# Optimization experiments

Measured on AMD Instinct MI355X. Metric: run time of the kernel, lower is better.

Reference implementation:

```python
import jax, jax.numpy as jnp
import numpy as np

B, S, E = 4, 2048, 512
H = 8          # 'layers' = number of heads
DK, DV = 64, 64
DK_H, DV_H = DK // H, DV // H  # = 8 each


def setup_inputs() -> dict:
    key = jax.random.key(0)
    ks = jax.random.split(key, 8)
    scale = 1.0 / np.sqrt(E)
    return {
        "query": jax.random.normal(ks[0], (B, S, E), jnp.float32),
        "key": jax.random.normal(ks[1], (B, S, E), jnp.float32),
        "value": jax.random.normal(ks[2], (B, S, E), jnp.float32),
        "padding_mask": jnp.ones((B, S, S), dtype=bool),
        "decoder_mask": 1,
        # stacked per-head projection weights (nn.Linear, bias=False)
        "Wq": jax.random.normal(ks[3], (H, E, DK_H), jnp.float32) * scale,
        "Wk": jax.random.normal(ks[4], (H, E, DK_H), jnp.float32) * scale,
        "Wv": jax.random.normal(ks[5], (H, E, DV_H), jnp.float32) * scale,
        # output projection: Linear(dV -> embed_size) with bias
        "Wo": jax.random.normal(ks[6], (DV, E), jnp.float32) * (1.0 / np.sqrt(DV)),
        "bo": jax.random.normal(ks[7], (E,), jnp.float32) * 0.01,
    }


def reference(query, key, value, padding_mask, decoder_mask, Wq, Wk, Wv, Wo, bo):
    # Batched over all heads at once (same math as the per-head Python loop).
    Q = jnp.einsum("bse,hed->bhsd", query, Wq)   # [B,H,S,dk_h]
    K = jnp.einsum("bse,hed->bhsd", key, Wk)
    V = jnp.einsum("bse,hed->bhsd", value, Wv)
    s = jnp.einsum("bhsd,bhtd->bhst", Q, K)      # [B,H,S,S] raw scores
    if decoder_mask:
        # faithful to: where(tril(scores)==0.0, -inf, scores)
        s = jnp.where(jnp.tril(s) == 0.0, -jnp.inf, s)
    # masked_fill(~padding_mask, -inf), broadcast over heads
    s = jnp.where(padding_mask[:, None, :, :], s, -jnp.inf)
    # note: scaling happens AFTER masking in the original (-inf stays -inf)
    s = s / jnp.sqrt(jnp.float32(DK_H))
    a = jax.nn.softmax(s, axis=-1)
    # dropout in eval mode -> identity
    o = jnp.einsum("bhst,bhtd->bhsd", a, V)      # [B,H,S,dv_h]
    o = o.transpose(0, 2, 1, 3).reshape(o.shape[0], o.shape[2], H * DV_H)  # concat heads
    return o @ Wo + bo                            # output projection (dropout = identity)
```

## Files before the change

kernel.cpp:

```cpp
#include <hip/hip_runtime.h>

#define BB 4
#define SS 2048
#define EE 512
#define HH 8
#define DHH 8
#define DVV 64

#define NEG (-1e30f)

__global__ __launch_bounds__(256)
void proj_kernel(const float* __restrict__ q, const float* __restrict__ k,
                 const float* __restrict__ v,
                 const float* __restrict__ Wq, const float* __restrict__ Wk,
                 const float* __restrict__ Wv,
                 float* __restrict__ Qp, float* __restrict__ Kp,
                 float* __restrict__ Vp)
{
  const float* x; const float* W; float* outp;
  if (blockIdx.y == 0)      { x = q; W = Wq; outp = Qp; }
  else if (blockIdx.y == 1) { x = k; W = Wk; outp = Kp; }
  else                      { x = v; W = Wv; outp = Vp; }

  __shared__ float Xs[64][68];
  __shared__ float Ws[64][68];

  int t = threadIdx.x;
  int row0 = blockIdx.x * 64;
  int tr = t >> 4;
  int tc = t & 15;

  float acc[4][4];
  #pragma unroll
  for (int i = 0; i < 4; i++)
    #pragma unroll
    for (int j = 0; j < 4; j++) acc[i][j] = 0.f;

  for (int kt = 0; kt < EE/64; kt++) {
    __syncthreads();
    {
      int row = t >> 2;
      #pragma unroll
      for (int it = 0; it < 4; it++) {
        int kq = 4*it + (t & 3);
        float4 vv = *(const float4*)(x + (size_t)(row0+row)*EE + kt*64 + 4*kq);
        Xs[4*kq+0][row] = vv.x;
        Xs[4*kq+1][row] = vv.y;
        Xs[4*kq+2][row] = vv.z;
        Xs[4*kq+3][row] = vv.w;
      }
    }
    #pragma unroll
    for (int it = 0; it < 4; it++) {
      int lin = t + 256*it;
      int kk  = lin >> 4;
      int rem = lin & 15;
      int h   = rem >> 1;
      int dq  = rem & 1;
      float4 vv = *(const float4*)(W + (size_t)h*EE*DHH + (size_t)(kt*64+kk)*DHH + dq*4);
      *(float4*)&Ws[kk][h*8 + dq*4] = vv;
    }
    __syncthreads();

    #pragma unroll 8
    for (int kk = 0; kk < 64; kk++) {
      float4 a = *(const float4*)&Xs[kk][4*tr];
      float4 bq = *(const float4*)&Ws[kk][4*tc];
      float av[4] = {a.x, a.y, a.z, a.w};
      float bv[4] = {bq.x, bq.y, bq.z, bq.w};
      #pragma unroll
      for (int i = 0; i < 4; i++)
        #pragma unroll
        for (int j = 0; j < 4; j++) acc[i][j] += av[i] * bv[j];
    }
  }

  int h = tc >> 1, dbase = (tc & 1) * 4;
  #pragma unroll
  for (int i = 0; i < 4; i++) {
    int row = row0 + 4*tr + i;
    int b = row >> 11, s = row & (SS - 1);
    float4 vv; vv.x = acc[i][0]; vv.y = acc[i][1]; vv.z = acc[i][2]; vv.w = acc[i][3];
    *(float4*)(outp + (((size_t)b*HH + h)*SS + s)*DHH + dbase) = vv;
  }
}

__global__ __launch_bounds__(256, 2)
void attn_kernel(const float* __restrict__ Qp, const float* __restrict__ Kp,
                 const float* __restrict__ Vp, float* __restrict__ O)
{
  int bx = blockIdx.x, h = blockIdx.y, b = blockIdx.z;
  const float* Qh = Qp + (((size_t)b*HH + h)*SS)*DHH;
  const float* Kh = Kp + (((size_t)b*HH + h)*SS)*DHH;
  const float* Vh = Vp + (((size_t)b*HH + h)*SS)*DHH;

  __shared__ float Ks[2][128*DHH];
  __shared__ float Vs[2][128*DHH];
  __shared__ float Ps[4*64*10];

  const int t  = threadIdx.x;
  const int rg = t & 15;
  const int cs = t >> 4;
  const float SCL = 0.35355339059327373f * 1.4426950408889634f;

  int cur = 0;

  for (int pass = 0; pass < 2; pass++) {
    const int qb = (pass == 0) ? bx : (31 - bx);
    const int row0t = qb*64 + 4*rg;

    float qreg[4][8];
    #pragma unroll
    for (int i = 0; i < 4; i++) {
      const float* qp = Qh + (size_t)(row0t + i) * DHH;
      float4 a = *(const float4*)qp;
      float4 c = *(const float4*)(qp + 4);
      qreg[i][0] = a.x*SCL; qreg[i][1] = a.y*SCL;
      qreg[i][2] = a.z*SCL; qreg[i][3] = a.w*SCL;
      qreg[i][4] = c.x*SCL; qreg[i][5] = c.y*SCL;
      qreg[i][6] = c.z*SCL; qreg[i][7] = c.w*SCL;
    }

    float M = 0.f, negM = 0.f;
    float l[4];
    float o[4][8];
    #pragma unroll
    for (int i = 0; i < 4; i++) {
      l[i] = 0.f;
      #pragma unroll
      for (int d = 0; d < 8; d++) o[i][d] = 0.f;
    }

    ((float4*)Ks[cur])[t] = ((const float4*)Kh)[t];
    ((float4*)Vs[cur])[t] = ((const float4*)Vh)[t];

    const int ktd = qb >> 1;
    for (int kt = 0; kt <= ktd; kt++) {
      __syncthreads();
      float4 kstg, vstg;
      const bool pre = (kt < ktd);
      if (pre) {
        kstg = ((const float4*)(Kh + (size_t)(kt+1)*128*DHH))[t];
        vstg = ((const float4*)(Vh + (size_t)(kt+1)*128*DHH))[t];
      }
      const float* KsC = Ks[cur];
      const float* VsC = Vs[cur];

      if (kt < ktd) {
        #pragma unroll
        for (int j = 0; j < 8; j++) {
          const int c8 = (cs + 16*j) * DHH;
          float4 k0 = *(const float4*)&KsC[c8];
          float4 k1 = *(const float4*)&KsC[c8 + 4];
          float4 v0 = *(const float4*)&VsC[c8];
          float4 v1 = *(const float4*)&VsC[c8 + 4];
          #pragma unroll
          for (int i = 0; i < 4; i++) {
            float s = fmaf(qreg[i][0], k0.x, negM);
            s = fmaf(qreg[i][1], k0.y, s);
            s = fmaf(qreg[i][2], k0.z, s);
            s = fmaf(qreg[i][3], k0.w, s);
            s = fmaf(qreg[i][4], k1.x, s);
            s = fmaf(qreg[i][5], k1.y, s);
            s = fmaf(qreg[i][6], k1.z, s);
            s = fmaf(qreg[i][7], k1.w, s);
            const float p = __builtin_amdgcn_exp2f(s);
            l[i] += p;
            o[i][0] = fmaf(p, v0.x, o[i][0]);
            o[i][1] = fmaf(p, v0.y, o[i][1]);
            o[i][2] = fmaf(p, v0.z, o[i][2]);
            o[i][3] = fmaf(p, v0.w, o[i][3]);
            o[i][4] = fmaf(p, v1.x, o[i][4]);
            o[i][5] = fmaf(p, v1.y, o[i][5]);
            o[i][6] = fmaf(p, v1.z, o[i][6]);
            o[i][7] = fmaf(p, v1.w, o[i][7]);
          }
        }
      } else {
        #pragma unroll
        for (int j = 0; j < 8; j++) {
          const int c  = cs + 16*j;
          const int cg = kt*128 + c;
          if (cg > row0t + 3) break;
          const int c8 = c * DHH;
          float4 k0 = *(const float4*)&KsC[c8];
          float4 k1 = *(const float4*)&KsC[c8 + 4];
          float4 v0 = *(const float4*)&VsC[c8];
          float4 v1 = *(const float4*)&VsC[c8 + 4];
          #pragma unroll
          for (int i = 0; i < 4; i++) {
            float s = fmaf(qreg[i][0], k0.x, negM);
            s = fmaf(qreg[i][1], k0.y, s);
            s = fmaf(qreg[i][2], k0.z, s);
            s = fmaf(qreg[i][3], k0.w, s);
            s = fmaf(qreg[i][4], k1.x, s);
            s = fmaf(qreg[i][5], k1.y, s);
            s = fmaf(qreg[i][6], k1.z, s);
            s = fmaf(qreg[i][7], k1.w, s);
            s = (cg > row0t + i) ? NEG : s;
            const float p = __builtin_amdgcn_exp2f(s);
            l[i] += p;
            o[i][0] = fmaf(p, v0.x, o[i][0]);
            o[i][1] = fmaf(p, v0.y, o[i][1]);
            o[i][2] = fmaf(p, v0.z, o[i][2]);
            o[i][3] = fmaf(p, v0.w, o[i][3]);
            o[i][4] = fmaf(p, v1.x, o[i][4]);
            o[i][5] = fmaf(p, v1.y, o[i][5]);
            o[i][6] = fmaf(p, v1.z, o[i][6]);
            o[i][7] = fmaf(p, v1.w, o[i][7]);
          }
        }
      }

      float lm = fmaxf(fmaxf(l[0], l[1]), fmaxf(l[2], l[3]));
      if (__any(lm > 1e18f)) {
        const float dsc = 5.421010862427522e-20f;
        #pragma unroll
        for (int i = 0; i < 4; i++) {
          l[i] *= dsc;
          #pragma unroll
          for (int d = 0; d < 8; d++) o[i][d] *= dsc;
        }
        M += 64.f; negM = -M;
      }

      if (pre) {
        ((float4*)Ks[cur ^ 1])[t] = kstg;
        ((float4*)Vs[cur ^ 1])[t] = vstg;
        cur ^= 1;
      }
    }

    #pragma unroll
    for (int i = 0; i < 4; i++) {
      l[i] += __shfl_xor(l[i], 16);
      #pragma unroll
      for (int d = 0; d < 8; d++) o[i][d] += __shfl_xor(o[i][d], 16);
      l[i] += __shfl_xor(l[i], 32);
      #pragma unroll
      for (int d = 0; d < 8; d++) o[i][d] += __shfl_xor(o[i][d], 32);
    }

    if ((t & 48) == 0) {
      const int w = t >> 6;
      #pragma unroll
      for (int i = 0; i < 4; i++) {
        float* ps = &Ps[(size_t)(w*64 + 4*rg + i) * 10];
        ps[0] = M; ps[1] = l[i];
        #pragma unroll
        for (int d = 0; d < 8; d++) ps[2 + d] = o[i][d];
      }
    }
    __syncthreads();

    if (t < 64) {
      float Mx = NEG, L = 0.f;
      float O8[8] = {0,0,0,0,0,0,0,0};
      #pragma unroll
      for (int ww = 0; ww < 4; ww++) {
        const float* ps = &Ps[(size_t)(ww*64 + t) * 10];
        const float mo = ps[0], lo = ps[1];
        const float mm = fmaxf(Mx, mo);
        const float a1 = __builtin_amdgcn_exp2f(Mx - mm);
        const float a2 = __builtin_amdgcn_exp2f(mo - mm);
        L = L*a1 + lo*a2;
        #pragma unroll
        for (int d = 0; d < 8; d++) O8[d] = O8[d]*a1 + ps[2 + d]*a2;
        Mx = mm;
      }
      const float inv = 1.0f / L;
      const int qrow = qb*64 + t;
      float* dst = O + ((size_t)b*SS + qrow)*DVV + h*DHH;
      float4 w0, w1;
      w0.x = O8[0]*inv; w0.y = O8[1]*inv; w0.z = O8[2]*inv; w0.w = O8[3]*inv;
      w1.x = O8[4]*inv; w1.y = O8[5]*inv; w1.z = O8[6]*inv; w1.w = O8[7]*inv;
      *(float4*)dst = w0;
      *(float4*)(dst + 4) = w1;
    }
  }
}

__global__ __launch_bounds__(256)
void outproj_kernel(const float* __restrict__ Oin, const float* __restrict__ Wo,
                    const float* __restrict__ bo, float* __restrict__ out)
{
  __shared__ float Os[64][68];
  int t = threadIdx.x;
  int row0 = blockIdx.x * 64;
  int col0 = blockIdx.y * 128;

  {
    int row = t >> 2;
    #pragma unroll
    for (int it = 0; it < 4; it++) {
      int kq = 4*it + (t & 3);
      float4 vv = *(const float4*)(Oin + (size_t)(row0+row)*DVV + 4*kq);
      Os[4*kq+0][row] = vv.x;
      Os[4*kq+1][row] = vv.y;
      Os[4*kq+2][row] = vv.z;
      Os[4*kq+3][row] = vv.w;
    }
  }
  __syncthreads();

  int rg = t >> 5;
  int tc = t & 31;
  const float* wp = Wo + col0 + 4*tc;
  float4 b4 = *(const float4*)(bo + col0 + 4*tc);

  float acc[8][4];
  #pragma unroll
  for (int r = 0; r < 8; r++) {
    acc[r][0] = b4.x; acc[r][1] = b4.y; acc[r][2] = b4.z; acc[r][3] = b4.w;
  }

  #pragma unroll 8
  for (int k = 0; k < DVV; k++) {
    float4 w = *(const float4*)(wp + (size_t)k*EE);
    float xr[8];
    *(float4*)&xr[0] = *(const float4*)&Os[k][8*rg];
    *(float4*)&xr[4] = *(const float4*)&Os[k][8*rg + 4];
    #pragma unroll
    for (int r = 0; r < 8; r++) {
      acc[r][0] += xr[r]*w.x;
      acc[r][1] += xr[r]*w.y;
      acc[r][2] += xr[r]*w.z;
      acc[r][3] += xr[r]*w.w;
    }
  }

  #pragma unroll
  for (int r = 0; r < 8; r++) {
    int row = row0 + 8*rg + r;
    float4 vv; vv.x = acc[r][0]; vv.y = acc[r][1]; vv.z = acc[r][2]; vv.w = acc[r][3];
    *(float4*)(out + (size_t)row*EE + col0 + 4*tc) = vv;
  }
}

extern "C" void kernel_launch(void* const* d_in, const int* in_sizes, int n_in,
                              void* d_out, int out_size, void* d_ws, size_t ws_size,
                              hipStream_t stream) {
  const void* qkv[3] = {nullptr, nullptr, nullptr};
  const void* Wlist[4] = {nullptr, nullptr, nullptr, nullptr};
  const void* bo = nullptr;
  int nqkv = 0, nw = 0;
  for (int i = 0; i < n_in; i++) {
    int sz = in_sizes[i];
    if (sz == BB*SS*EE)            { if (nqkv < 3) qkv[nqkv] = d_in[i]; nqkv++; }
    else if (sz == HH*EE*DHH)      { if (nw < 4) Wlist[nw] = d_in[i]; nw++; }
    else if (sz == EE)             { bo = d_in[i]; }
  }
  float* out = (float*)d_out;

  float* Qp = (float*)d_ws;
  float* Kp = Qp + (size_t)BB*HH*SS*DHH;
  float* Vp = Kp + (size_t)BB*HH*SS*DHH;
  float* O  = Vp + (size_t)BB*HH*SS*DHH;

  dim3 gA(BB*SS/64, 3, 1);
  proj_kernel<<<gA, 256, 0, stream>>>((const float*)qkv[0], (const float*)qkv[1],
                                      (const float*)qkv[2],
                                      (const float*)Wlist[0], (const float*)Wlist[1],
                                      (const float*)Wlist[2], Qp, Kp, Vp);

  dim3 gB(16, HH, BB);
  attn_kernel<<<gB, 256, 0, stream>>>(Qp, Kp, Vp, O);

  dim3 gC(BB*SS/64, EE/128, 1);
  outproj_kernel<<<gC, 256, 0, stream>>>(O, (const float*)Wlist[3],
                                         (const float*)bo, out);
}
```

Baseline: 220.7 us.

## Double-buffer projection GEMM tiles and remap threads to row-per-lane layout

The projection kernel now double-buffers its X and W shared-memory tiles, prefetching the next k-tile into registers while computing on the current one. The per-thread mapping also changes: each lane owns one row and each wave computes 16 output columns. The wave reads W as a broadcast and writes two full 8-float head outputs per thread. This hides global-load latency and drops one barrier per iteration, at the cost of doubled LDS use and more registers.

```diff
diff --git a/kernel.cpp b/kernel.cpp
--- a/kernel.cpp
+++ b/kernel.cpp
@@ -22,67 +22,122 @@
   else if (blockIdx.y == 1) { x = k; W = Wk; outp = Kp; }
   else                      { x = v; W = Wv; outp = Vp; }
 
-  __shared__ float Xs[64][68];
-  __shared__ float Ws[64][68];
-
-  int t = threadIdx.x;
-  int row0 = blockIdx.x * 64;
-  int tr = t >> 4;
-  int tc = t & 15;
-
-  float acc[4][4];
+  __shared__ float Xs[2][64][68];
+  __shared__ float Ws[2][64][68];
+
+  const int t    = threadIdx.x;
+  const int lane = t & 63;
+  const int wv   = t >> 6;
+  const int row0 = blockIdx.x * 64;
+
+  const int srow = t >> 2;
+
+  float acc[16];
   #pragma unroll
-  for (int i = 0; i < 4; i++)
-    #pragma unroll
-    for (int j = 0; j < 4; j++) acc[i][j] = 0.f;
-
+  for (int i = 0; i < 16; i++) acc[i] = 0.f;
+
+  float4 xv[4], wvv[4];
+
+  #pragma unroll
+  for (int it = 0; it < 4; it++) {
+    int kq = 4*it + (t & 3);
+    xv[it] = *(const float4*)(x + (size_t)(row0 + srow)*EE + 4*kq);
+    int lin = t + 256*it;
+    int kk  = lin >> 4;
+    int rem = lin & 15;
+    int h   = rem >> 1;
+    int dq  = rem & 1;
+    wvv[it] = *(const float4*)(W + (size_t)h*EE*DHH + (size_t)kk*DHH + dq*4);
+  }
+  #pragma unroll
+  for (int it = 0; it < 4; it++) {
+    int kq = 4*it + (t & 3);
+    Xs[0][4*kq+0][srow] = xv[it].x;
+    Xs[0][4*kq+1][srow] = xv[it].y;
+    Xs[0][4*kq+2][srow] = xv[it].z;
+    Xs[0][4*kq+3][srow] = xv[it].w;
+    int lin = t + 256*it;
+    int kk  = lin >> 4;
+    int rem = lin & 15;
+    int h   = rem >> 1;
+    int dq  = rem & 1;
+    *(float4*)&Ws[0][kk][h*8 + dq*4] = wvv[it];
+  }
+
+  int cur = 0;
   for (int kt = 0; kt < EE/64; kt++) {
     __syncthreads();
-    {
-      int row = t >> 2;
+    const bool pre = (kt < EE/64 - 1);
+    if (pre) {
       #pragma unroll
       for (int it = 0; it < 4; it++) {
         int kq = 4*it + (t & 3);
-        float4 vv = *(const float4*)(x + (size_t)(row0+row)*EE + kt*64 + 4*kq);
-        Xs[4*kq+0][row] = vv.x;
-        Xs[4*kq+1][row] = vv.y;
-        Xs[4*kq+2][row] = vv.z;
-        Xs[4*kq+3][row] = vv.w;
-      }
-    }
-    #pragma unroll
-    for (int it = 0; it < 4; it++) {
-      int lin = t + 256*it;
-      int kk  = lin >> 4;
-      int rem = lin & 15;
-      int h   = rem >> 1;
-      int dq  = rem & 1;
-      float4 vv = *(const float4*)(W + (size_t)h*EE*DHH + (size_t)(kt*64+kk)*DHH + dq*4);
-      *(float4*)&Ws[kk][h*8 + dq*4] = vv;
-    }
-    __syncthreads();
+        xv[it] = *(const float4*)(x + (size_t)(row0 + srow)*EE + (kt+1)*64 + 4*kq);
+        int lin = t + 256*it;
+        int kk  = lin >> 4;
+        int rem = lin & 15;
+        int h   = rem >> 1;
+        int dq  = rem & 1;
+        wvv[it] = *(const float4*)(W + (size_t)h*EE*DHH + (size_t)((kt+1)*64 + kk)*DHH + dq*4);
+      }
+    }
 
     #pragma unroll 8
     for (int kk = 0; kk < 64; kk++) {
-      float4 a = *(const float4*)&Xs[kk][4*tr];
-      float4 bq = *(const float4*)&Ws[kk][4*tc];
-      float av[4] = {a.x, a.y, a.z, a.w};
-      float bv[4] = {bq.x, bq.y, bq.z, bq.w};
-      #pragma unroll
-      for (int i = 0; i < 4; i++)
-        #pragma unroll
-        for (int j = 0; j < 4; j++) acc[i][j] += av[i] * bv[j];
-    }
-  }
-
-  int h = tc >> 1, dbase = (tc & 1) * 4;
-  #pragma unroll
-  for (int i = 0; i < 4; i++) {
-    int row = row0 + 4*tr + i;
-    int b = row >> 11, s = row & (SS - 1);
-    float4 vv; vv.x = acc[i][0]; vv.y = acc[i][1]; vv.z = acc[i][2]; vv.w = acc[i][3];
-    *(float4*)(outp + (((size_t)b*HH + h)*SS + s)*DHH + dbase) = vv;
-  }
+      float a = Xs[cur][kk][lane];
+      float4 w0 = *(const float4*)&Ws[cur][kk][16*wv + 0];
+      float4 w1 = *(const float4*)&Ws[cur][kk][16*wv + 4];
+      float4 w2 = *(const float4*)&Ws[cur][kk][16*wv + 8];
+      float4 w3 = *(const float4*)&Ws[cur][kk][16*wv + 12];
+      acc[0]  = fmaf(a, w0.x, acc[0]);
+      acc[1]  = fmaf(a, w0.y, acc[1]);
+      acc[2]  = fmaf(a, w0.z, acc[2]);
+      acc[3]  = fmaf(a, w0.w, acc[3]);
+      acc[4]  = fmaf(a, w1.x, acc[4]);
+      acc[5]  = fmaf(a, w1.y, acc[5]);
+      acc[6]  = fmaf(a, w1.z, acc[6]);
+      acc[7]  = fmaf(a, w1.w, acc[7]);
+      acc[8]  = fmaf(a, w2.x, acc[8]);
+      acc[9]  = fmaf(a, w2.y, acc[9]);
+      acc[10] = fmaf(a, w2.z, acc[10]);
+      acc[11] = fmaf(a, w2.w, acc[11]);
+      acc[12] = fmaf(a, w3.x, acc[12]);
+      acc[13] = fmaf(a, w3.y, acc[13]);
+      acc[14] = fmaf(a, w3.z, acc[14]);
+      acc[15] = fmaf(a, w3.w, acc[15]);
+    }
+
+    if (pre) {
+      #pragma unroll
+      for (int it = 0; it < 4; it++) {
+        int kq = 4*it + (t & 3);
+        Xs[cur^1][4*kq+0][srow] = xv[it].x;
+        Xs[cur^1][4*kq+1][srow] = xv[it].y;
+        Xs[cur^1][4*kq+2][srow] = xv[it].z;
+        Xs[cur^1][4*kq+3][srow] = xv[it].w;
+        int lin = t + 256*it;
+        int kk  = lin >> 4;
+        int rem = lin & 15;
+        int h   = rem >> 1;
+        int dq  = rem & 1;
+        *(float4*)&Ws[cur^1][kk][h*8 + dq*4] = wvv[it];
+      }
+      cur ^= 1;
+    }
+  }
+
+  const int grow = row0 + lane;
+  const int b = grow >> 11, s = grow & (SS - 1);
+  const int h0 = 2*wv, h1 = 2*wv + 1;
+  float* p0 = outp + (((size_t)b*HH + h0)*SS + s)*DHH;
+  float* p1 = outp + (((size_t)b*HH + h1)*SS + s)*DHH;
+  float4 o0, o1, o2, o3;
+  o0.x = acc[0];  o0.y = acc[1];  o0.z = acc[2];  o0.w = acc[3];
+  o1.x = acc[4];  o1.y = acc[5];  o1.z = acc[6];  o1.w = acc[7];
+  o2.x = acc[8];  o2.y = acc[9];  o2.z = acc[10]; o2.w = acc[11];
+  o3.x = acc[12]; o3.y = acc[13]; o3.z = acc[14]; o3.w = acc[15];
+  *(float4*)p0 = o0; *(float4*)(p0 + 4) = o1;
+  *(float4*)p1 = o2; *(float4*)(p1 + 4) = o3;
 }
 
 __global__ __launch_bounds__(256, 2)
```

Measured after the change: 229.3 us. 3.9% more time.

## Double-buffer X tile in projection kernel and read weights directly from global

Applied to the files above, without the earlier changes.

In the QKV projection kernel, the X tile is now double-buffered in shared memory with register prefetch of the next K-slice, so global loads overlap with compute and one barrier per iteration is removed. The weight tile is no longer staged in shared memory; each thread reads its float4 of weights straight from global (L1/L2 cached) inside the inner loop. This trades shared-memory traffic and a barrier for more global/cache load instructions in the hot loop. The projection is a small share of the total time next to attention, so the overall effect is likely limited.

```diff
diff --git a/kernel.cpp b/kernel.cpp
--- a/kernel.cpp
+++ b/kernel.cpp
@@ -22,13 +22,15 @@
   else if (blockIdx.y == 1) { x = k; W = Wk; outp = Kp; }
   else                      { x = v; W = Wv; outp = Vp; }
 
-  __shared__ float Xs[64][68];
-  __shared__ float Ws[64][68];
-
-  int t = threadIdx.x;
-  int row0 = blockIdx.x * 64;
-  int tr = t >> 4;
-  int tc = t & 15;
+  __shared__ float Xs[2][64][68];
+
+  const int t    = threadIdx.x;
+  const int row0 = blockIdx.x * 64;
+  const int tr = t >> 4;
+  const int tc = t & 15;
+  const int srow = t >> 2;
+
+  const float* wp = W + (size_t)(tc >> 1)*EE*DHH + (size_t)(tc & 1)*4;
 
   float acc[4][4];
   #pragma unroll
@@ -36,46 +38,72 @@
     #pragma unroll
     for (int j = 0; j < 4; j++) acc[i][j] = 0.f;
 
+  float4 xv[4];
+
+  #pragma unroll
+  for (int it = 0; it < 4; it++) {
+    int kq = 4*it + (t & 3);
+    xv[it] = *(const float4*)(x + (size_t)(row0 + srow)*EE + 4*kq);
+  }
+  #pragma unroll
+  for (int it = 0; it < 4; it++) {
+    int kq = 4*it + (t & 3);
+    Xs[0][4*kq+0][srow] = xv[it].x;
+    Xs[0][4*kq+1][srow] = xv[it].y;
+    Xs[0][4*kq+2][srow] = xv[it].z;
+    Xs[0][4*kq+3][srow] = xv[it].w;
+  }
+
+  int cur = 0;
   for (int kt = 0; kt < EE/64; kt++) {
     __syncthreads();
-    {
-      int row = t >> 2;
+    const bool pre = (kt < EE/64 - 1);
+    if (pre) {
       #pragma unroll
       for (int it = 0; it < 4; it++) {
         int kq = 4*it + (t & 3);
-        float4 vv = *(const float4*)(x + (size_t)(row0+row)*EE + kt*64 + 4*kq);
-        Xs[4*kq+0][row] = vv.x;
-        Xs[4*kq+1][row] = vv.y;
-        Xs[4*kq+2][row] = vv.z;
-        Xs[4*kq+3][row] = vv.w;
-      }
-    }
-    #pragma unroll
-    for (int it = 0; it < 4; it++) {
-      int lin = t + 256*it;
-      int kk  = lin >> 4;
-      int rem = lin & 15;
-      int h   = rem >> 1;
-      int dq  = rem & 1;
-      float4 vv = *(const float4*)(W + (size_t)h*EE*DHH + (size_t)(kt*64+kk)*DHH + dq*4);
-      *(float4*)&Ws[kk][h*8 + dq*4] = vv;
-    }
-    __syncthreads();
-
+        xv[it] = *(const float4*)(x + (size_t)(row0 + srow)*EE + (kt+1)*64 + 4*kq);
+      }
+    }
+
+    const float* wk = wp + (size_t)(kt*64)*DHH;
     #pragma unroll 8
     for (int kk = 0; kk < 64; kk++) {
-      float4 a = *(const float4*)&Xs[kk][4*tr];
-      float4 bq = *(const float4*)&Ws[kk][4*tc];
+      float4 a = *(const float4*)&Xs[cur][kk][4*tr];
+      float4 w = *(const float4*)(wk + (size_t)kk*DHH);
       float av[4] = {a.x, a.y, a.z, a.w};
-      float bv[4] = {bq.x, bq.y, bq.z, bq.w};
-      #pragma unroll
-      for (int i = 0; i < 4; i++)
-        #pragma unroll
-        for (int j = 0; j < 4; j++) acc[i][j] += av[i] * bv[j];
-    }
-  }
-
-  int h = tc >> 1, dbase = (tc & 1) * 4;
+      acc[0][0] = fmaf(av[0], w.x, acc[0][0]);
+      acc[0][1] = fmaf(av[0], w.y, acc[0][1]);
+      acc[0][2] = fmaf(av[0], w.z, acc[0][2]);
+      acc[0][3] = fmaf(av[0], w.w, acc[0][3]);
+      acc[1][0] = fmaf(av[1], w.x, acc[1][0]);
+      acc[1][1] = fmaf(av[1], w.y, acc[1][1]);
+      acc[1][2] = fmaf(av[1], w.z, acc[1][2]);
+      acc[1][3] = fmaf(av[1], w.w, acc[1][3]);
+      acc[2][0] = fmaf(av[2], w.x, acc[2][0]);
+      acc[2][1] = fmaf(av[2], w.y, acc[2][1]);
+      acc[2][2] = fmaf(av[2], w.z, acc[2][2]);
+      acc[2][3] = fmaf(av[2], w.w, acc[2][3]);
+      acc[3][0] = fmaf(av[3], w.x, acc[3][0]);
+      acc[3][1] = fmaf(av[3], w.y, acc[3][1]);
+      acc[3][2] = fmaf(av[3], w.z, acc[3][2]);
+      acc[3][3] = fmaf(av[3], w.w, acc[3][3]);
+    }
+
+    if (pre) {
+      #pragma unroll
+      for (int it = 0; it < 4; it++) {
+        int kq = 4*it + (t & 3);
+        Xs[cur^1][4*kq+0][srow] = xv[it].x;
+        Xs[cur^1][4*kq+1][srow] = xv[it].y;
+        Xs[cur^1][4*kq+2][srow] = xv[it].z;
+        Xs[cur^1][4*kq+3][srow] = xv[it].w;
+      }
+      cur ^= 1;
+    }
+  }
+
+  const int h = tc >> 1, dbase = (tc & 1) * 4;
   #pragma unroll
   for (int i = 0; i < 4; i++) {
     int row = row0 + 4*tr + i;
```

Result: slower. 251.4 us (+13.9%).

## Fuse projection, attention and output projection into one persistent kernel with grid barriers

Applied to the files above, without the earlier changes.

Merges the three kernel launches into a single 512-block kernel that runs the QKV projection, causal attention and output projection in turn, separated by atomic-counter grid barriers. Shared memory is overlaid through a union, and a memset clears the counter before each launch. The aim is to remove the launch gaps and tail effects between stages. In exchange it adds global barrier spin cost, relies on all 512 blocks being co-resident (2 per CU on 256 CUs) or it can deadlock, and adds a memset call.

```diff
diff --git a/kernel.cpp b/kernel.cpp
--- a/kernel.cpp
+++ b/kernel.cpp
@@ -9,331 +9,349 @@
 
 #define NEG (-1e30f)
 
-__global__ __launch_bounds__(256)
-void proj_kernel(const float* __restrict__ q, const float* __restrict__ k,
-                 const float* __restrict__ v,
-                 const float* __restrict__ Wq, const float* __restrict__ Wk,
-                 const float* __restrict__ Wv,
-                 float* __restrict__ Qp, float* __restrict__ Kp,
-                 float* __restrict__ Vp)
+
+union SharedU {
+  struct { float Xs[64][68]; float Ws[64][68]; } pj;
+  struct { float Ks[2][128*DHH]; float Vs[2][128*DHH]; float Ps[4*64*10]; } at;
+  struct { float Os[64][68]; } op;
+};
+
+__device__ __forceinline__ void grid_barrier(unsigned* cnt, unsigned target) {
+  __syncthreads();
+  if (threadIdx.x == 0) {
+    __hip_atomic_fetch_add(cnt, 1u, __ATOMIC_ACQ_REL, __HIP_MEMORY_SCOPE_AGENT);
+    unsigned v;
+    do {
+      __builtin_amdgcn_s_sleep(2);
+      v = __hip_atomic_load(cnt, __ATOMIC_ACQUIRE, __HIP_MEMORY_SCOPE_AGENT);
+    } while (v < target);
+  }
+  __syncthreads();
+}
+
+__global__ __launch_bounds__(256, 2)
+void fused_kernel(const float* __restrict__ q, const float* __restrict__ k,
+                  const float* __restrict__ v,
+                  const float* __restrict__ Wq, const float* __restrict__ Wk,
+                  const float* __restrict__ Wv,
+                  const float* __restrict__ Wo, const float* __restrict__ bo,
+                  float* __restrict__ Qp, float* __restrict__ Kp,
+                  float* __restrict__ Vp, float* __restrict__ O,
+                  float* __restrict__ out, unsigned* __restrict__ cnt)
 {
-  const float* x; const float* W; float* outp;
-  if (blockIdx.y == 0)      { x = q; W = Wq; outp = Qp; }
-  else if (blockIdx.y == 1) { x = k; W = Wk; outp = Kp; }
-  else                      { x = v; W = Wv; outp = Vp; }
-
-  __shared__ float Xs[64][68];
-  __shared__ float Ws[64][68];
-
-  int t = threadIdx.x;
-  int row0 = blockIdx.x * 64;
-  int tr = t >> 4;
-  int tc = t & 15;
-
-  float acc[4][4];
-  #pragma unroll
-  for (int i = 0; i < 4; i++)
+  __shared__ SharedU sh;
+  const int bid = blockIdx.x;
+  const int t   = threadIdx.x;
+
+  if (bid < 384) {
+    const int mat = bid >> 7;
+    const float* x; const float* W; float* outp;
+    if (mat == 0)      { x = q; W = Wq; outp = Qp; }
+    else if (mat == 1) { x = k; W = Wk; outp = Kp; }
+    else               { x = v; W = Wv; outp = Vp; }
+
+    const int row0 = (bid & 127) * 64;
+    const int tr = t >> 4;
+    const int tc = t & 15;
+
+    float acc[4][4];
     #pragma unroll
-    for (int j = 0; j < 4; j++) acc[i][j] = 0.f;
-
-  for (int kt = 0; kt < EE/64; kt++) {
-    __syncthreads();
+    for (int i = 0; i < 4; i++)
+      #pragma unroll
+      for (int j = 0; j < 4; j++) acc[i][j] = 0.f;
+
+    for (int kt = 0; kt < EE/64; kt++) {
+      __syncthreads();
+      {
+        int row = t >> 2;
+        #pragma unroll
+        for (int it = 0; it < 4; it++) {
+          int kq = 4*it + (t & 3);
+          float4 vv = *(const float4*)(x + (size_t)(row0+row)*EE + kt*64 + 4*kq);
+          sh.pj.Xs[4*kq+0][row] = vv.x;
+          sh.pj.Xs[4*kq+1][row] = vv.y;
+          sh.pj.Xs[4*kq+2][row] = vv.z;
+          sh.pj.Xs[4*kq+3][row] = vv.w;
+        }
+      }
+      #pragma unroll
+      for (int it = 0; it < 4; it++) {
+        int lin = t + 256*it;
+        int kk  = lin >> 4;
+        int rem = lin & 15;
+        int h   = rem >> 1;
+        int dq  = rem & 1;
+        float4 vv = *(const float4*)(W + (size_t)h*EE*DHH + (size_t)(kt*64+kk)*DHH + dq*4);
+        *(float4*)&sh.pj.Ws[kk][h*8 + dq*4] = vv;
+      }
+      __syncthreads();
+
+      #pragma unroll 8
+      for (int kk = 0; kk < 64; kk++) {
+        float4 a  = *(const float4*)&sh.pj.Xs[kk][4*tr];
+        float4 bq = *(const float4*)&sh.pj.Ws[kk][4*tc];
+        float av[4] = {a.x, a.y, a.z, a.w};
+        float bv[4] = {bq.x, bq.y, bq.z, bq.w};
+        #pragma unroll
+        for (int i = 0; i < 4; i++)
+          #pragma unroll
+          for (int j = 0; j < 4; j++) acc[i][j] += av[i] * bv[j];
+      }
+    }
+
+    const int h = tc >> 1, dbase = (tc & 1) * 4;
+    #pragma unroll
+    for (int i = 0; i < 4; i++) {
+      int row = row0 + 4*tr + i;
+      int b = row >> 11, s = row & (SS - 1);
+      float4 vv; vv.x = acc[i][0]; vv.y = acc[i][1]; vv.z = acc[i][2]; vv.w = acc[i][3];
+      *(float4*)(outp + (((size_t)b*HH + h)*SS + s)*DHH + dbase) = vv;
+    }
+  }
+
+  grid_barrier(cnt, 512);
+
+  {
+    const int bx = bid & 15;
+    const int h  = (bid >> 4) & 7;
+    const int b  = bid >> 7;
+    const float* Qh = Qp + (((size_t)b*HH + h)*SS)*DHH;
+    const float* Kh = Kp + (((size_t)b*HH + h)*SS)*DHH;
+    const float* Vh = Vp + (((size_t)b*HH + h)*SS)*DHH;
+
+    const int rg = t & 15;
+    const int cs = t >> 4;
+    const float SCL = 0.35355339059327373f * 1.4426950408889634f;
+
+    int cur = 0;
+
+    for (int pass = 0; pass < 2; pass++) {
+      const int qb = (pass == 0) ? bx : (31 - bx);
+      const int row0t = qb*64 + 4*rg;
+
+      float qreg[4][8];
+      #pragma unroll
+      for (int i = 0; i < 4; i++) {
+        const float* qp = Qh + (size_t)(row0t + i) * DHH;
+        float4 a = *(const float4*)qp;
+        float4 c = *(const float4*)(qp + 4);
+        qreg[i][0] = a.x*SCL; qreg[i][1] = a.y*SCL;
+        qreg[i][2] = a.z*SCL; qreg[i][3] = a.w*SCL;
+        qreg[i][4] = c.x*SCL; qreg[i][5] = c.y*SCL;
+        qreg[i][6] = c.z*SCL; qreg[i][7] = c.w*SCL;
+      }
+
+      float M = 0.f, negM = 0.f;
+      float l[4];
+      float o[4][8];
+      #pragma unroll
+      for (int i = 0; i < 4; i++) {
+        l[i] = 0.f;
+        #pragma unroll
+        for (int d = 0; d < 8; d++) o[i][d] = 0.f;
+      }
+
+      ((float4*)sh.at.Ks[cur])[t] = ((const float4*)Kh)[t];
+      ((float4*)sh.at.Vs[cur])[t] = ((const float4*)Vh)[t];
+
+      const int ktd = qb >> 1;
+      for (int kt = 0; kt <= ktd; kt++) {
+        __syncthreads();
+        float4 kstg, vstg;
+        const bool pre = (kt < ktd);
+        if (pre) {
+          kstg = ((const float4*)(Kh + (size_t)(kt+1)*128*DHH))[t];
+          vstg = ((const float4*)(Vh + (size_t)(kt+1)*128*DHH))[t];
+        }
+        const float* KsC = sh.at.Ks[cur];
+        const float* VsC = sh.at.Vs[cur];
+
+        if (kt < ktd) {
+          #pragma unroll
+          for (int j = 0; j < 8; j++) {
+            const int c8 = (cs + 16*j) * DHH;
+            float4 k0 = *(const float4*)&KsC[c8];
+            float4 k1 = *(const float4*)&KsC[c8 + 4];
+            float4 v0 = *(const float4*)&VsC[c8];
+            float4 v1 = *(const float4*)&VsC[c8 + 4];
+            #pragma unroll
+            for (int i = 0; i < 4; i++) {
+              float s = fmaf(qreg[i][0], k0.x, negM);
+              s = fmaf(qreg[i][1], k0.y, s);
+              s = fmaf(qreg[i][2], k0.z, s);
+              s = fmaf(qreg[i][3], k0.w, s);
+              s = fmaf(qreg[i][4], k1.x, s);
+              s = fmaf(qreg[i][5], k1.y, s);
+              s = fmaf(qreg[i][6], k1.z, s);
+              s = fmaf(qreg[i][7], k1.w, s);
+              const float p = __builtin_amdgcn_exp2f(s);
+              l[i] += p;
+              o[i][0] = fmaf(p, v0.x, o[i][0]);
+              o[i][1] = fmaf(p, v0.y, o[i][1]);
+              o[i][2] = fmaf(p, v0.z, o[i][2]);
+              o[i][3] = fmaf(p, v0.w, o[i][3]);
+              o[i][4] = fmaf(p, v1.x, o[i][4]);
+              o[i][5] = fmaf(p, v1.y, o[i][5]);
+              o[i][6] = fmaf(p, v1.z, o[i][6]);
+              o[i][7] = fmaf(p, v1.w, o[i][7]);
+            }
+          }
+        } else {
+          #pragma unroll
+          for (int j = 0; j < 8; j++) {
+            const int c  = cs + 16*j;
+            const int cg = kt*128 + c;
+            if (cg > row0t + 3) break;
+            const int c8 = c * DHH;
+            float4 k0 = *(const float4*)&KsC[c8];
+            float4 k1 = *(const float4*)&KsC[c8 + 4];
+            float4 v0 = *(const float4*)&VsC[c8];
+            float4 v1 = *(const float4*)&VsC[c8 + 4];
+            #pragma unroll
+            for (int i = 0; i < 4; i++) {
+              float s = fmaf(qreg[i][0], k0.x, negM);
+              s = fmaf(qreg[i][1], k0.y, s);
+              s = fmaf(qreg[i][2], k0.z, s);
+              s = fmaf(qreg[i][3], k0.w, s);
+              s = fmaf(qreg[i][4], k1.x, s);
+              s = fmaf(qreg[i][5], k1.y, s);
+              s = fmaf(qreg[i][6], k1.z, s);
+              s = fmaf(qreg[i][7], k1.w, s);
+              s = (cg > row0t + i) ? NEG : s;
+              const float p = __builtin_amdgcn_exp2f(s);
+              l[i] += p;
+              o[i][0] = fmaf(p, v0.x, o[i][0]);
+              o[i][1] = fmaf(p, v0.y, o[i][1]);
+              o[i][2] = fmaf(p, v0.z, o[i][2]);
+              o[i][3] = fmaf(p, v0.w, o[i][3]);
+              o[i][4] = fmaf(p, v1.x, o[i][4]);
+              o[i][5] = fmaf(p, v1.y, o[i][5]);
+              o[i][6] = fmaf(p, v1.z, o[i][6]);
+              o[i][7] = fmaf(p, v1.w, o[i][7]);
+            }
+          }
+        }
+
+        float lm = fmaxf(fmaxf(l[0], l[1]), fmaxf(l[2], l[3]));
+        if (__any(lm > 1e18f)) {
+          const float dsc = 5.421010862427522e-20f;
+          #pragma unroll
+          for (int i = 0; i < 4; i++) {
+            l[i] *= dsc;
+            #pragma unroll
+            for (int d = 0; d < 8; d++) o[i][d] *= dsc;
+          }
+          M += 64.f; negM = -M;
+        }
+
+        if (pre) {
+          ((float4*)sh.at.Ks[cur ^ 1])[t] = kstg;
+          ((float4*)sh.at.Vs[cur ^ 1])[t] = vstg;
+          cur ^= 1;
+        }
+      }
+
+      #pragma unroll
+      for (int i = 0; i < 4; i++) {
+        l[i] += __shfl_xor(l[i], 16);
+        #pragma unroll
+        for (int d = 0; d < 8; d++) o[i][d] += __shfl_xor(o[i][d], 16);
+        l[i] += __shfl_xor(l[i], 32);
+        #pragma unroll
+        for (int d = 0; d < 8; d++) o[i][d] += __shfl_xor(o[i][d], 32);
+      }
+
+      if ((t & 48) == 0) {
+        const int w = t >> 6;
+        #pragma unroll
+        for (int i = 0; i < 4; i++) {
+          float* ps = &sh.at.Ps[(size_t)(w*64 + 4*rg + i) * 10];
+          ps[0] = M; ps[1] = l[i];
+          #pragma unroll
+          for (int d = 0; d < 8; d++) ps[2 + d] = o[i][d];
+        }
+      }
+      __syncthreads();
+
+      if (t < 64) {
+        float Mx = NEG, L = 0.f;
+        float O8[8] = {0,0,0,0,0,0,0,0};
+        #pragma unroll
+        for (int ww = 0; ww < 4; ww++) {
+          const float* ps = &sh.at.Ps[(size_t)(ww*64 + t) * 10];
+          const float mo = ps[0], lo = ps[1];
+          const float mm = fmaxf(Mx, mo);
+          const float a1 = __builtin_amdgcn_exp2f(Mx - mm);
+          const float a2 = __builtin_amdgcn_exp2f(mo - mm);
+          L = L*a1 + lo*a2;
+          #pragma unroll
+          for (int d = 0; d < 8; d++) O8[d] = O8[d]*a1 + ps[2 + d]*a2;
+          Mx = mm;
+        }
+        const float inv = 1.0f / L;
+        const int qrow = qb*64 + t;
+        float* dst = O + ((size_t)b*SS + qrow)*DVV + h*DHH;
+        float4 w0, w1;
+        w0.x = O8[0]*inv; w0.y = O8[1]*inv; w0.z = O8[2]*inv; w0.w = O8[3]*inv;
+        w1.x = O8[4]*inv; w1.y = O8[5]*inv; w1.z = O8[6]*inv; w1.w = O8[7]*inv;
+        *(float4*)dst = w0;
+        *(float4*)(dst + 4) = w1;
+      }
+    }
+  }
+
+  grid_barrier(cnt, 1024);
+
+  {
+    const int row0 = (bid & 127) * 64;
+    const int col0 = (bid >> 7) * 128;
+
     {
       int row = t >> 2;
       #pragma unroll
       for (int it = 0; it < 4; it++) {
         int kq = 4*it + (t & 3);
-        float4 vv = *(const float4*)(x + (size_t)(row0+row)*EE + kt*64 + 4*kq);
-        Xs[4*kq+0][row] = vv.x;
-        Xs[4*kq+1][row] = vv.y;
-        Xs[4*kq+2][row] = vv.z;
-        Xs[4*kq+3][row] = vv.w;
-      }
-    }
-    #pragma unroll
-    for (int it = 0; it < 4; it++) {
-      int lin = t + 256*it;
-      int kk  = lin >> 4;
-      int rem = lin & 15;
-      int h   = rem >> 1;
-      int dq  = rem & 1;
-      float4 vv = *(const float4*)(W + (size_t)h*EE*DHH + (size_t)(kt*64+kk)*DHH + dq*4);
-      *(float4*)&Ws[kk][h*8 + dq*4] = vv;
+        float4 vv = *(const float4*)(O + (size_t)(row0+row)*DVV + 4*kq);
+        sh.op.Os[4*kq+0][row] = vv.x;
+        sh.op.Os[4*kq+1][row] = vv.y;
+        sh.op.Os[4*kq+2][row] = vv.z;
+        sh.op.Os[4*kq+3][row] = vv.w;
+      }
     }
     __syncthreads();
 
-    #pragma unroll 8
-    for (int kk = 0; kk < 64; kk++) {
-      float4 a = *(const float4*)&Xs[kk][4*tr];
-      float4 bq = *(const float4*)&Ws[kk][4*tc];
-      float av[4] = {a.x, a.y, a.z, a.w};
-      float bv[4] = {bq.x, bq.y, bq.z, bq.w};
-      #pragma unroll
-      for (int i = 0; i < 4; i++)
-        #pragma unroll
-        for (int j = 0; j < 4; j++) acc[i][j] += av[i] * bv[j];
-    }
-  }
-
-  int h = tc >> 1, dbase = (tc & 1) * 4;
-  #pragma unroll
-  for (int i = 0; i < 4; i++) {
-    int row = row0 + 4*tr + i;
-    int b = row >> 11, s = row & (SS - 1);
-    float4 vv; vv.x = acc[i][0]; vv.y = acc[i][1]; vv.z = acc[i][2]; vv.w = acc[i][3];
-    *(float4*)(outp + (((size_t)b*HH + h)*SS + s)*DHH + dbase) = vv;
-  }
-}
-
-__global__ __launch_bounds__(256, 2)
-void attn_kernel(const float* __restrict__ Qp, const float* __restrict__ Kp,
-                 const float* __restrict__ Vp, float* __restrict__ O)
-{
-  int bx = blockIdx.x, h = blockIdx.y, b = blockIdx.z;
-  const float* Qh = Qp + (((size_t)b*HH + h)*SS)*DHH;
-  const float* Kh = Kp + (((size_t)b*HH + h)*SS)*DHH;
-  const float* Vh = Vp + (((size_t)b*HH + h)*SS)*DHH;
-
-  __shared__ float Ks[2][128*DHH];
-  __shared__ float Vs[2][128*DHH];
-  __shared__ float Ps[4*64*10];
-
-  const int t  = threadIdx.x;
-  const int rg = t & 15;
-  const int cs = t >> 4;
-  const float SCL = 0.35355339059327373f * 1.4426950408889634f;
-
-  int cur = 0;
-
-  for (int pass = 0; pass < 2; pass++) {
-    const int qb = (pass == 0) ? bx : (31 - bx);
-    const int row0t = qb*64 + 4*rg;
-
-    float qreg[4][8];
-    #pragma unroll
-    for (int i = 0; i < 4; i++) {
-      const float* qp = Qh + (size_t)(row0t + i) * DHH;
-      float4 a = *(const float4*)qp;
-      float4 c = *(const float4*)(qp + 4);
-      qreg[i][0] = a.x*SCL; qreg[i][1] = a.y*SCL;
-      qreg[i][2] = a.z*SCL; qreg[i][3] = a.w*SCL;
-      qreg[i][4] = c.x*SCL; qreg[i][5] = c.y*SCL;
-      qreg[i][6] = c.z*SCL; qreg[i][7] = c.w*SCL;
-    }
-
-    float M = 0.f, negM = 0.f;
-    float l[4];
-    float o[4][8];
-    #pragma unroll
-    for (int i = 0; i < 4; i++) {
-      l[i] = 0.f;
-      #pragma unroll
-      for (int d = 0; d < 8; d++) o[i][d] = 0.f;
-    }
-
-    ((float4*)Ks[cur])[t] = ((const float4*)Kh)[t];
-    ((float4*)Vs[cur])[t] = ((const float4*)Vh)[t];
-
-    const int ktd = qb >> 1;
-    for (int kt = 0; kt <= ktd; kt++) {
-      __syncthreads();
-      float4 kstg, vstg;
-      const bool pre = (kt < ktd);
-      if (pre) {
-        kstg = ((const float4*)(Kh + (size_t)(kt+1)*128*DHH))[t];
-        vstg = ((const float4*)(Vh + (size_t)(kt+1)*128*DHH))[t];
-      }
-      const float* KsC = Ks[cur];
-      const float* VsC = Vs[cur];
-
-      if (kt < ktd) {
-        #pragma unroll
-        for (int j = 0; j < 8; j++) {
-          const int c8 = (cs + 16*j) * DHH;
-          float4 k0 = *(const float4*)&KsC[c8];
-          float4 k1 = *(const float4*)&KsC[c8 + 4];
-          float4 v0 = *(const float4*)&VsC[c8];
-          float4 v1 = *(const float4*)&VsC[c8 + 4];
-          #pragma unroll
-          for (int i = 0; i < 4; i++) {
-            float s = fmaf(qreg[i][0], k0.x, negM);
-            s = fmaf(qreg[i][1], k0.y, s);
-            s = fmaf(qreg[i][2], k0.z, s);
-            s = fmaf(qreg[i][3], k0.w, s);
-            s = fmaf(qreg[i][4], k1.x, s);
-            s = fmaf(qreg[i][5], k1.y, s);
-            s = fmaf(qreg[i][6], k1.z, s);
-            s = fmaf(qreg[i][7], k1.w, s);
-            const float p = __builtin_amdgcn_exp2f(s);
-            l[i] += p;
-            o[i][0] = fmaf(p, v0.x, o[i][0]);
-            o[i][1] = fmaf(p, v0.y, o[i][1]);
-            o[i][2] = fmaf(p, v0.z, o[i][2]);
-            o[i][3] = fmaf(p, v0.w, o[i][3]);
-            o[i][4] = fmaf(p, v1.x, o[i][4]);
-            o[i][5] = fmaf(p, v1.y, o[i][5]);
-            o[i][6] = fmaf(p, v1.z, o[i][6]);
-            o[i][7] = fmaf(p, v1.w, o[i][7]);
-          }
-        }
-      } else {
-        #pragma unroll
-        for (int j = 0; j < 8; j++) {
-          const int c  = cs + 16*j;
-          const int cg = kt*128 + c;
-          if (cg > row0t + 3) break;
-          const int c8 = c * DHH;
-          float4 k0 = *(const float4*)&KsC[c8];
-          float4 k1 = *(const float4*)&KsC[c8 + 4];
-          float4 v0 = *(const float4*)&VsC[c8];
-          float4 v1 = *(const float4*)&VsC[c8 + 4];
-          #pragma unroll
-          for (int i = 0; i < 4; i++) {
-            float s = fmaf(qreg[i][0], k0.x, negM);
-            s = fmaf(qreg[i][1], k0.y, s);
-            s = fmaf(qreg[i][2], k0.z, s);
-            s = fmaf(qreg[i][3], k0.w, s);
-            s = fmaf(qreg[i][4], k1.x, s);
-            s = fmaf(qreg[i][5], k1.y, s);
-            s = fmaf(qreg[i][6], k1.z, s);
-            s = fmaf(qreg[i][7], k1.w, s);
-            s = (cg > row0t + i) ? NEG : s;
-            const float p = __builtin_amdgcn_exp2f(s);
-            l[i] += p;
-            o[i][0] = fmaf(p, v0.x, o[i][0]);
-            o[i][1] = fmaf(p, v0.y, o[i][1]);
-            o[i][2] = fmaf(p, v0.z, o[i][2]);
-            o[i][3] = fmaf(p, v0.w, o[i][3]);
-            o[i][4] = fmaf(p, v1.x, o[i][4]);
-            o[i][5] = fmaf(p, v1.y, o[i][5]);
-            o[i][6] = fmaf(p, v1.z, o[i][6]);
-            o[i][7] = fmaf(p, v1.w, o[i][7]);
-          }
-        }
-      }
-
-      float lm = fmaxf(fmaxf(l[0], l[1]), fmaxf(l[2], l[3]));
-      if (__any(lm > 1e18f)) {
-        const float dsc = 5.421010862427522e-20f;
-        #pragma unroll
-        for (int i = 0; i < 4; i++) {
-          l[i] *= dsc;
-          #pragma unroll
-          for (int d = 0; d < 8; d++) o[i][d] *= dsc;
-        }
-        M += 64.f; negM = -M;
-      }
-
-      if (pre) {
-        ((float4*)Ks[cur ^ 1])[t] = kstg;
-        ((float4*)Vs[cur ^ 1])[t] = vstg;
-        cur ^= 1;
-      }
-    }
-
-    #pragma unroll
-    for (int i = 0; i < 4; i++) {
-      l[i] += __shfl_xor(l[i], 16);
-      #pragma unroll
-      for (int d = 0; d < 8; d++) o[i][d] += __shfl_xor(o[i][d], 16);
-      l[i] += __shfl_xor(l[i], 32);
-      #pragma unroll
-      for (int d = 0; d < 8; d++) o[i][d] += __shfl_xor(o[i][d], 32);
-    }
-
-    if ((t & 48) == 0) {
-      const int w = t >> 6;
-      #pragma unroll
-      for (int i = 0; i < 4; i++) {
-        float* ps = &Ps[(size_t)(w*64 + 4*rg + i) * 10];
-        ps[0] = M; ps[1] = l[i];
-        #pragma unroll
-        for (int d = 0; d < 8; d++) ps[2 + d] = o[i][d];
-      }
-    }
-    __syncthreads();
-
-    if (t < 64) {
-      float Mx = NEG, L = 0.f;
-      float O8[8] = {0,0,0,0,0,0,0,0};
-      #pragma unroll
-      for (int ww = 0; ww < 4; ww++) {
-        const float* ps = &Ps[(size_t)(ww*64 + t) * 10];
-        const float mo = ps[0], lo = ps[1];
-        const float mm = fmaxf(Mx, mo);
-        const float a1 = __builtin_amdgcn_exp2f(Mx - mm);
-        const float a2 = __builtin_amdgcn_exp2f(mo - mm);
-        L = L*a1 + lo*a2;
-        #pragma unroll
-        for (int d = 0; d < 8; d++) O8[d] = O8[d]*a1 + ps[2 + d]*a2;
-        Mx = mm;
-      }
-      const float inv = 1.0f / L;
-      const int qrow = qb*64 + t;
-      float* dst = O + ((size_t)b*SS + qrow)*DVV + h*DHH;
-      float4 w0, w1;
-      w0.x = O8[0]*inv; w0.y = O8[1]*inv; w0.z = O8[2]*inv; w0.w = O8[3]*inv;
-      w1.x = O8[4]*inv; w1.y = O8[5]*inv; w1.z = O8[6]*inv; w1.w = O8[7]*inv;
-      *(float4*)dst = w0;
-      *(float4*)(dst + 4) = w1;
-    }
-  }
-}
-
-__global__ __launch_bounds__(256)
-void outproj_kernel(const float* __restrict__ Oin, const float* __restrict__ Wo,
-                    const float* __restrict__ bo, float* __restrict__ out)
-{
-  __shared__ float Os[64][68];
-  int t = threadIdx.x;
-  int row0 = blockIdx.x * 64;
-  int col0 = blockIdx.y * 128;
-
-  {
-    int row = t >> 2;
-    #pragma unroll
-    for (int it = 0; it < 4; it++) {
-      int kq = 4*it + (t & 3);
-      float4 vv = *(const float4*)(Oin + (size_t)(row0+row)*DVV + 4*kq);
-      Os[4*kq+0][row] = vv.x;
-      Os[4*kq+1][row] = vv.y;
-      Os[4*kq+2][row] = vv.z;
-      Os[4*kq+3][row] = vv.w;
-    }
-  }
-  __syncthreads();
-
-  int rg = t >> 5;
-  int tc = t & 31;
-  const float* wp = Wo + col0 + 4*tc;
-  float4 b4 = *(const float4*)(bo + col0 + 4*tc);
-
-  float acc[8][4];
-  #pragma unroll
-  for (int r = 0; r < 8; r++) {
-    acc[r][0] = b4.x; acc[r][1] = b4.y; acc[r][2] = b4.z; acc[r][3] = b4.w;
-  }
-
-  #pragma unroll 8
-  for (int k = 0; k < DVV; k++) {
-    float4 w = *(const float4*)(wp + (size_t)k*EE);
-    float xr[8];
-    *(float4*)&xr[0] = *(const float4*)&Os[k][8*rg];
-    *(float4*)&xr[4] = *(const float4*)&Os[k][8*rg + 4];
+    int rg = t >> 5;
+    int tc = t & 31;
+    const float* wp = Wo + col0 + 4*tc;
+    float4 b4 = *(const float4*)(bo + col0 + 4*tc);
+
+    float acc[8][4];
     #pragma unroll
     for (int r = 0; r < 8; r++) {
-      acc[r][0] += xr[r]*w.x;
-      acc[r][1] += xr[r]*w.y;
-      acc[r][2] += xr[r]*w.z;
-      acc[r][3] += xr[r]*w.w;
-    }
-  }
-
-  #pragma unroll
-  for (int r = 0; r < 8; r++) {
-    int row = row0 + 8*rg + r;
-    float4 vv; vv.x = acc[r][0]; vv.y = acc[r][1]; vv.z = acc[r][2]; vv.w = acc[r][3];
-    *(float4*)(out + (size_t)row*EE + col0 + 4*tc) = vv;
+      acc[r][0] = b4.x; acc[r][1] = b4.y; acc[r][2] = b4.z; acc[r][3] = b4.w;
+    }
+
+    #pragma unroll 8
+    for (int kk = 0; kk < DVV; kk++) {
+      float4 w = *(const float4*)(wp + (size_t)kk*EE);
+      float xr[8];
+      *(float4*)&xr[0] = *(const float4*)&sh.op.Os[kk][8*rg];
+      *(float4*)&xr[4] = *(const float4*)&sh.op.Os[kk][8*rg + 4];
+      #pragma unroll
+      for (int r = 0; r < 8; r++) {
+        acc[r][0] += xr[r]*w.x;
+        acc[r][1] += xr[r]*w.y;
+        acc[r][2] += xr[r]*w.z;
+        acc[r][3] += xr[r]*w.w;
+      }
+    }
+
+    #pragma unroll
+    for (int r = 0; r < 8; r++) {
+      int row = row0 + 8*rg + r;
+      float4 vv; vv.x = acc[r][0]; vv.y = acc[r][1]; vv.z = acc[r][2]; vv.w = acc[r][3];
+      *(float4*)(out + (size_t)row*EE + col0 + 4*tc) = vv;
+    }
   }
 }
 
@@ -356,17 +374,13 @@
   float* Kp = Qp + (size_t)BB*HH*SS*DHH;
   float* Vp = Kp + (size_t)BB*HH*SS*DHH;
   float* O  = Vp + (size_t)BB*HH*SS*DHH;
-
-  dim3 gA(BB*SS/64, 3, 1);
-  proj_kernel<<<gA, 256, 0, stream>>>((const float*)qkv[0], (const float*)qkv[1],
-                                      (const float*)qkv[2],
-                                      (const float*)Wlist[0], (const float*)Wlist[1],
-                                      (const float*)Wlist[2], Qp, Kp, Vp);
-
-  dim3 gB(16, HH, BB);
-  attn_kernel<<<gB, 256, 0, stream>>>(Qp, Kp, Vp, O);
-
-  dim3 gC(BB*SS/64, EE/128, 1);
-  outproj_kernel<<<gC, 256, 0, stream>>>(O, (const float*)Wlist[3],
-                                         (const float*)bo, out);
+  unsigned* cnt = (unsigned*)((char*)d_ws + (size_t)8*1024*1024);
+
+  hipMemsetAsync(cnt, 0, sizeof(unsigned), stream);
+
+  fused_kernel<<<dim3(512), dim3(256), 0, stream>>>(
+      (const float*)qkv[0], (const float*)qkv[1], (const float*)qkv[2],
+      (const float*)Wlist[0], (const float*)Wlist[1], (const float*)Wlist[2],
+      (const float*)Wlist[3], (const float*)bo,
+      Qp, Kp, Vp, O, out, cnt);
 }
```

Result: slower. 355.7 us (+61.2%).
